# Optimization experiments

Hardware: AMD Instinct MI355X
Metric: run time of the kernel (lower is better)

The kernel has to match this reference:

```python
import jax, jax.numpy as jnp
import numpy as np

# Qwen3 MoE sparse block reference.
# E experts, top-k routing with softmax probs, normalized top-k weights,
# gated-SiLU expert MLPs (gate/up H->I, down I->H), weighted scatter-combine.
E, K, H, I = 8, 2, 2048, 768
B, S = 2, 2048


def setup_inputs() -> dict:
    key = jax.random.key(0)
    k0, k1, k2, k3, k4 = jax.random.split(key, 5)
    hidden_states = jax.random.normal(k0, (B, S, H), jnp.float32)
    w_router = jax.random.normal(k1, (H, E), jnp.float32) * (1.0 / np.sqrt(H))
    wi0 = jax.random.normal(k2, (E, H, I), jnp.float32) * 0.02  # gate proj
    wi1 = jax.random.normal(k3, (E, H, I), jnp.float32) * 0.02  # up proj
    wo = jax.random.normal(k4, (E, I, H), jnp.float32) * 0.02   # down proj
    return {"hidden_states": hidden_states, "w_router": w_router,
            "wi0": wi0, "wi1": wi1, "wo": wo}


def _moe(hidden_states, w_router, wi0, wi1, wo):
    b, s, h = hidden_states.shape
    x = hidden_states.reshape(-1, h)                       # [T, H]
    router_logits = x @ w_router                           # [T, E]
    probs = jax.nn.softmax(router_logits.astype(jnp.float32), axis=-1)
    top_w, top_i = jax.lax.top_k(probs, K)                 # [T, K]
    # norm_topk_prob = True
    top_w = top_w / jnp.sum(top_w, axis=-1, keepdims=True)
    top_w = top_w.astype(x.dtype)
    # per-(expert, token) combine weight; zero for unrouted pairs -> same math
    # as the original gather/MLP/scatter-add over selected tokens.
    onehot = jax.nn.one_hot(top_i, E, dtype=x.dtype)       # [T, K, E]
    comb = jnp.einsum('tk,tke->et', top_w, onehot)         # [E, T]
    g = jax.nn.silu(jnp.einsum('th,ehi->eti', x, wi0))     # [E, T, I]
    u = jnp.einsum('th,ehi->eti', x, wi1)                  # [E, T, I]
    y = jnp.einsum('eti,eih->eth', g * u, wo)              # [E, T, H]
    out = jnp.einsum('et,eth->th', comb, y)                # [T, H]
    return out.reshape(b, s, h), router_logits


def reference(hidden_states, w_router, wi0, wi1, wo):
    return _moe(hidden_states, w_router, wi0, wi1, wo)
```

## Files before the change

### kernel.cpp

```cpp
#include <hip/hip_runtime.h>

#define T_TOK 4096
#define H_DIM 2048
#define I_DIM 768
#define E_NUM 8

typedef __attribute__((ext_vector_type(8))) short bf16x8;
typedef __attribute__((ext_vector_type(4))) float f32x4;

__device__ __forceinline__ unsigned short f2bf(float f) {
  union { float f; unsigned int u; } c; c.f = f;
  unsigned int r = c.u + 0x7fffu + ((c.u >> 16) & 1u);
  return (unsigned short)(r >> 16);
}

__device__ __forceinline__ void gl_lds16(const unsigned short* g, unsigned short* l) {
  __builtin_amdgcn_global_load_lds(
      (const __attribute__((address_space(1))) unsigned int*)g,
      (__attribute__((address_space(3))) unsigned int*)l, 16, 0, 0);
}

__global__ __launch_bounds__(256) void transpose_cast_kernel(
    const float* __restrict__ src, unsigned short* __restrict__ dst,
    int K, int N)
{
  const int e = blockIdx.z;
  const int kb = blockIdx.y * 64, nb = blockIdx.x * 64;
  src += (size_t)e * K * N + (size_t)kb * N + nb;
  dst += (size_t)e * N * K + (size_t)nb * K + kb;
  __shared__ float tile[64][65];
  const int tid = threadIdx.x;
  const int lr = tid >> 4, lc = (tid & 15) * 4;
#pragma unroll
  for (int it = 0; it < 4; ++it) {
    float4 v = *(const float4*)(src + (size_t)(lr + it * 16) * N + lc);
    tile[lr + it * 16][lc]     = v.x;
    tile[lr + it * 16][lc + 1] = v.y;
    tile[lr + it * 16][lc + 2] = v.z;
    tile[lr + it * 16][lc + 3] = v.w;
  }
  __syncthreads();
  const int wn = tid >> 2, wk = (tid & 3) * 16;
  union { uint4 u[2]; unsigned short h[16]; } o;
#pragma unroll
  for (int j = 0; j < 16; ++j) o.h[j] = f2bf(tile[wk + j][wn]);
  *(uint4*)(dst + (size_t)wn * K + wk)     = o.u[0];
  *(uint4*)(dst + (size_t)wn * K + wk + 8) = o.u[1];
}

#define RTOK 8
__global__ __launch_bounds__(256) void router_kernel(
    const float* __restrict__ x,
    const float* __restrict__ wr,
    unsigned short* __restrict__ xbf,
    float* __restrict__ logits_out,
    int* __restrict__ counts,
    int* __restrict__ entries,
    float* __restrict__ entry_w)
{
  const int tid = threadIdx.x;
  const int w = tid >> 6, lane = tid & 63;
  const int t0 = blockIdx.x * RTOK;
  const int hb = w * 512 + lane * 8;

  float wreg[8][8];
#pragma unroll
  for (int r = 0; r < 8; ++r) {
    *(float4*)&wreg[r][0] = *(const float4*)(wr + (size_t)(hb + r) * E_NUM);
    *(float4*)&wreg[r][4] = *(const float4*)(wr + (size_t)(hb + r) * E_NUM + 4);
  }

  __shared__ float red[RTOK][4][E_NUM];
  __shared__ float lg[RTOK][E_NUM];
  __shared__ int   ch_i[RTOK][2];
  __shared__ float ch_w[RTOK][2];

  for (int tt = 0; tt < RTOK; ++tt) {
    const int t = t0 + tt;
    float xv[8];
    *(float4*)&xv[0] = *(const float4*)(x + (size_t)t * H_DIM + hb);
    *(float4*)&xv[4] = *(const float4*)(x + (size_t)t * H_DIM + hb + 4);
    union { uint4 u; unsigned short h[8]; } o;
#pragma unroll
    for (int j = 0; j < 8; ++j) o.h[j] = f2bf(xv[j]);
    *(uint4*)(xbf + (size_t)t * H_DIM + hb) = o.u;

    float acc[E_NUM];
#pragma unroll
    for (int e = 0; e < E_NUM; ++e) acc[e] = 0.f;
#pragma unroll
    for (int r = 0; r < 8; ++r)
#pragma unroll
      for (int e = 0; e < E_NUM; ++e) acc[e] = fmaf(xv[r], wreg[r][e], acc[e]);
#pragma unroll
    for (int off = 32; off > 0; off >>= 1)
#pragma unroll
      for (int e = 0; e < E_NUM; ++e) acc[e] += __shfl_down(acc[e], off);
    if (lane == 0)
#pragma unroll
      for (int e = 0; e < E_NUM; ++e) red[tt][w][e] = acc[e];
  }
  __syncthreads();

  if (tid < RTOK * E_NUM) {
    const int tt = tid >> 3, e = tid & 7;
    float l = red[tt][0][e] + red[tt][1][e] + red[tt][2][e] + red[tt][3][e];
    lg[tt][e] = l;
    logits_out[(size_t)(t0 + tt) * E_NUM + e] = l;
  }
  __syncthreads();

  if (tid < RTOK) {
    const int tt = tid;
    float m1 = lg[tt][0]; int i1 = 0;
#pragma unroll
    for (int e = 1; e < E_NUM; ++e) if (lg[tt][e] > m1) { m1 = lg[tt][e]; i1 = e; }
    float m2 = -3.4e38f; int i2 = -1;
#pragma unroll
    for (int e = 0; e < E_NUM; ++e) if (e != i1 && lg[tt][e] > m2) { m2 = lg[tt][e]; i2 = e; }
    float w1 = 1.f / (1.f + __expf(m2 - m1));
    ch_i[tt][0] = i1; ch_i[tt][1] = i2;
    ch_w[tt][0] = w1; ch_w[tt][1] = 1.f - w1;
  }
  __syncthreads();

  if (tid < E_NUM) {
    const int e = tid;
    int cnt = 0;
#pragma unroll
    for (int tt = 0; tt < RTOK; ++tt) {
      if (ch_i[tt][0] == e) ++cnt;
      if (ch_i[tt][1] == e) ++cnt;
    }
    if (cnt > 0) {
      int base = atomicAdd(&counts[e], cnt);
      int pos = 0;
#pragma unroll
      for (int tt = 0; tt < RTOK; ++tt) {
#pragma unroll
        for (int k = 0; k < 2; ++k) {
          if (ch_i[tt][k] == e) {
            entries[e * T_TOK + base + pos] = (t0 + tt) * 2 + k;
            entry_w[e * T_TOK + base + pos] = ch_w[tt][k];
            ++pos;
          }
        }
      }
    }
  }
}

#define FRAG(arr, row, cb) \
  (*(const bf16x8*)(&(arr)[((row) << 6) + ((((cb)) ^ ((row) & 7)) << 3)]))

__global__ __launch_bounds__(256) void moe_up_kernel(
    const unsigned short* __restrict__ xbf,
    const unsigned short* __restrict__ wgt,
    const unsigned short* __restrict__ wut,
    const int* __restrict__ counts,
    const int* __restrict__ entries,
    unsigned short* __restrict__ act)
{
  const int e = blockIdx.z;
  const int cnt = counts[e];
  const int m0 = blockIdx.y * 128;
  if (m0 >= cnt) return;
  const int n0 = blockIdx.x * 64;
  const int tid = threadIdx.x;

  __shared__ __align__(16) unsigned short As[128 * 64];
  __shared__ __align__(16) unsigned short Bg[64 * 64];
  __shared__ __align__(16) unsigned short Bu[64 * 64];
  __shared__ int rowp[128];

  if (tid < 128) rowp[tid] = (m0 + tid < cnt) ? entries[e * T_TOK + m0 + tid] : -1;
  __syncthreads();

  const int w = tid >> 6, lane = tid & 63;
  const int lrow = lane >> 3, lchunk = lane & 7;
  const int jj = lchunk ^ lrow;

  const unsigned short* wg_e = wgt + (size_t)e * I_DIM * H_DIM + (size_t)n0 * H_DIM;
  const unsigned short* wu_e = wut + (size_t)e * I_DIM * H_DIM + (size_t)n0 * H_DIM;
  const unsigned short* gA[4];
  unsigned short* lA[4];
#pragma unroll
  for (int t4 = 0; t4 < 4; ++t4) {
    int r = (t4 * 4 + w) * 8 + lrow;
    int p = rowp[r];
    int tok = (p >= 0) ? (p >> 1) : 0;
    gA[t4] = xbf + (size_t)tok * H_DIM + jj * 8;
    lA[t4] = As + (t4 * 4 + w) * 512;
  }
  const unsigned short* gG[2]; const unsigned short* gU[2]; unsigned short* lG[2]; unsigned short* lU[2];
#pragma unroll
  for (int t2 = 0; t2 < 2; ++t2) {
    int r = (t2 * 4 + w) * 8 + lrow;
    gG[t2] = wg_e + (size_t)r * H_DIM + jj * 8;
    gU[t2] = wu_e + (size_t)r * H_DIM + jj * 8;
    lG[t2] = Bg + (t2 * 4 + w) * 512;
    lU[t2] = Bu + (t2 * 4 + w) * 512;
  }

  f32x4 accg[4][2], accu[4][2];
#pragma unroll
  for (int i = 0; i < 4; ++i)
#pragma unroll
    for (int j = 0; j < 2; ++j) {
      accg[i][j] = (f32x4){0.f, 0.f, 0.f, 0.f};
      accu[i][j] = (f32x4){0.f, 0.f, 0.f, 0.f};
    }

  const int msub = (w >> 1) * 64, nsub = (w & 1) * 32;
  const int fm = lane & 15, fq = lane >> 4;
  const int f7 = fm & 7;

  for (int kt = 0; kt < H_DIM; kt += 64) {
#pragma unroll
    for (int t4 = 0; t4 < 4; ++t4) gl_lds16(gA[t4] + kt, lA[t4]);
#pragma unroll
    for (int t2 = 0; t2 < 2; ++t2) {
      gl_lds16(gG[t2] + kt, lG[t2]);
      gl_lds16(gU[t2] + kt, lU[t2]);
    }
    __syncthreads();
#pragma unroll
    for (int ks = 0; ks < 64; ks += 32) {
      const int cb = (ks >> 3) + fq;
      bf16x8 a[4], bg[2], bu[2];
#pragma unroll
      for (int mi = 0; mi < 4; ++mi)
        a[mi] = FRAG(As, msub + mi * 16 + fm, cb);
#pragma unroll
      for (int ni = 0; ni < 2; ++ni) {
        bg[ni] = FRAG(Bg, nsub + ni * 16 + fm, cb);
        bu[ni] = FRAG(Bu, nsub + ni * 16 + fm, cb);
      }
#pragma unroll
      for (int mi = 0; mi < 4; ++mi)
#pragma unroll
        for (int ni = 0; ni < 2; ++ni) {
          accg[mi][ni] = __builtin_amdgcn_mfma_f32_16x16x32_bf16(a[mi], bg[ni], accg[mi][ni], 0, 0, 0);
          accu[mi][ni] = __builtin_amdgcn_mfma_f32_16x16x32_bf16(a[mi], bu[ni], accu[mi][ni], 0, 0, 0);
        }
    }
    __syncthreads();
  }
#pragma unroll
  for (int mi = 0; mi < 4; ++mi) {
#pragma unroll
    for (int r = 0; r < 4; ++r) {
      int ml = msub + mi * 16 + fq * 4 + r;
      int p = rowp[ml];
      if (p < 0) continue;
      size_t base = (size_t)p * I_DIM + n0 + nsub + fm;
#pragma unroll
      for (int ni = 0; ni < 2; ++ni) {
        float g = accg[mi][ni][r];
        float u = accu[mi][ni][r];
        float h = g / (1.f + __expf(-g)) * u;
        act[base + ni * 16] = f2bf(h);
      }
    }
  }
}

__global__ __launch_bounds__(256) void moe_down_kernel(
    const unsigned short* __restrict__ act,
    const unsigned short* __restrict__ wot,
    const int* __restrict__ counts,
    const int* __restrict__ entries,
    const float* __restrict__ entry_w,
    float* __restrict__ out)
{
  const int e = blockIdx.z;
  const int cnt = counts[e];
  const int m0 = blockIdx.y * 128;
  if (m0 >= cnt) return;
  const int n0 = blockIdx.x * 128;
  const int tid = threadIdx.x;

  __shared__ __align__(16) unsigned short As[128 * 64];
  __shared__ __align__(16) unsigned short Bt[128 * 64];
  __shared__ int rowp[128];
  __shared__ float roww[128];

  if (tid < 128) {
    int idx = m0 + tid;
    rowp[tid] = (idx < cnt) ? entries[e * T_TOK + idx] : -1;
    roww[tid] = (idx < cnt) ? entry_w[e * T_TOK + idx] : 0.f;
  }
  __syncthreads();

  const int w = tid >> 6, lane = tid & 63;
  const int lrow = lane >> 3, lchunk = lane & 7;
  const int jj = lchunk ^ lrow;

  const unsigned short* wo_e = wot + (size_t)e * H_DIM * I_DIM + (size_t)n0 * I_DIM;
  const unsigned short* gA[4]; unsigned short* lA[4];
  const unsigned short* gB[4]; unsigned short* lB[4];
#pragma unroll
  for (int t4 = 0; t4 < 4; ++t4) {
    int r = (t4 * 4 + w) * 8 + lrow;
    int p = rowp[r];
    int pr = (p >= 0) ? p : 0;
    gA[t4] = act + (size_t)pr * I_DIM + jj * 8;
    lA[t4] = As + (t4 * 4 + w) * 512;
    gB[t4] = wo_e + (size_t)r * I_DIM + jj * 8;
    lB[t4] = Bt + (t4 * 4 + w) * 512;
  }

  f32x4 acc[4][4];
#pragma unroll
  for (int i = 0; i < 4; ++i)
#pragma unroll
    for (int j = 0; j < 4; ++j) acc[i][j] = (f32x4){0.f, 0.f, 0.f, 0.f};

  const int msub = (w >> 1) * 64, nsub = (w & 1) * 64;
  const int fm = lane & 15, fq = lane >> 4;

  for (int kt = 0; kt < I_DIM; kt += 64) {
#pragma unroll
    for (int t4 = 0; t4 < 4; ++t4) {
      gl_lds16(gA[t4] + kt, lA[t4]);
      gl_lds16(gB[t4] + kt, lB[t4]);
    }
    __syncthreads();
#pragma unroll
    for (int ks = 0; ks < 64; ks += 32) {
      const int cb = (ks >> 3) + fq;
      bf16x8 a[4], b[4];
#pragma unroll
      for (int mi = 0; mi < 4; ++mi)
        a[mi] = FRAG(As, msub + mi * 16 + fm, cb);
#pragma unroll
      for (int ni = 0; ni < 4; ++ni)
        b[ni] = FRAG(Bt, nsub + ni * 16 + fm, cb);
#pragma unroll
      for (int mi = 0; mi < 4; ++mi)
#pragma unroll
        for (int ni = 0; ni < 4; ++ni)
          acc[mi][ni] = __builtin_amdgcn_mfma_f32_16x16x32_bf16(a[mi], b[ni], acc[mi][ni], 0, 0, 0);
    }
    __syncthreads();
  }
#pragma unroll
  for (int mi = 0; mi < 4; ++mi) {
#pragma unroll
    for (int r = 0; r < 4; ++r) {
      int ml = msub + mi * 16 + fq * 4 + r;
      int p = rowp[ml];
      if (p < 0) continue;
      float wt = roww[ml];
      float* dst = out + (size_t)(p >> 1) * H_DIM + n0 + nsub + fm;
#pragma unroll
      for (int ni = 0; ni < 4; ++ni)
        atomicAdd(dst + ni * 16, acc[mi][ni][r] * wt);
    }
  }
}

extern "C" void kernel_launch(void* const* d_in, const int* in_sizes, int n_in,
                              void* d_out, int out_size, void* d_ws, size_t ws_size,
                              hipStream_t stream) {
  const float* x   = (const float*)d_in[0];
  const float* wr  = (const float*)d_in[1];
  const float* wi0 = (const float*)d_in[2];
  const float* wi1 = (const float*)d_in[3];
  const float* wo  = (const float*)d_in[4];
  float* out = (float*)d_out;
  float* logits_out = out + (size_t)T_TOK * H_DIM;

  char* w = (char*)d_ws;
  int* counts    = (int*)w;
  int* entries   = (int*)(w + 64);
  float* entry_w = (float*)(w + 64 + (size_t)E_NUM * T_TOK * 4);
  size_t off = 64 + 2 * (size_t)E_NUM * T_TOK * 4;
  unsigned short* xbf = (unsigned short*)(w + off); off += (size_t)T_TOK * H_DIM * 2;
  unsigned short* wgt = (unsigned short*)(w + off); off += (size_t)E_NUM * H_DIM * I_DIM * 2;
  unsigned short* wut = (unsigned short*)(w + off); off += (size_t)E_NUM * H_DIM * I_DIM * 2;
  unsigned short* wot = (unsigned short*)(w + off); off += (size_t)E_NUM * H_DIM * I_DIM * 2;
  unsigned short* act = (unsigned short*)(w + off);

  hipMemsetAsync(d_out, 0, (size_t)T_TOK * H_DIM * sizeof(float), stream);
  hipMemsetAsync(counts, 0, 64, stream);
  transpose_cast_kernel<<<dim3(I_DIM / 64, H_DIM / 64, E_NUM), 256, 0, stream>>>(
      wi0, wgt, H_DIM, I_DIM);
  transpose_cast_kernel<<<dim3(I_DIM / 64, H_DIM / 64, E_NUM), 256, 0, stream>>>(
      wi1, wut, H_DIM, I_DIM);
  transpose_cast_kernel<<<dim3(H_DIM / 64, I_DIM / 64, E_NUM), 256, 0, stream>>>(
      wo, wot, I_DIM, H_DIM);
  router_kernel<<<T_TOK / RTOK, 256, 0, stream>>>(x, wr, xbf, logits_out, counts, entries, entry_w);
  moe_up_kernel<<<dim3(I_DIM / 64, T_TOK / 128, E_NUM), 256, 0, stream>>>(
      xbf, wgt, wut, counts, entries, act);
  moe_down_kernel<<<dim3(H_DIM / 128, T_TOK / 128, E_NUM), 256, 0, stream>>>(
      act, wot, counts, entries, entry_w, out);
}
```

Measured before the change: 413.9 us.

## Double-buffer LDS tiles in MoE up and down GEMM kernels

Both expert GEMM kernels now keep two LDS buffers for the A and B tiles. Each k-iteration issues the global-to-LDS loads for the next tile before running the MFMAs on the current one, with a prologue load before the loop. The aim is to hide global load latency behind matrix math instead of stalling at a barrier right after each load. In exchange LDS use per block roughly doubles to about 64KB, which may cut how many blocks fit on a CU.

Result: no change. 410.3 us (-0.9%).

```diff
diff --git a/kernel.cpp b/kernel.cpp
--- a/kernel.cpp
+++ b/kernel.cpp
@@ -168,9 +168,9 @@
   const int n0 = blockIdx.x * 64;
   const int tid = threadIdx.x;
 
-  __shared__ __align__(16) unsigned short As[128 * 64];
-  __shared__ __align__(16) unsigned short Bg[64 * 64];
-  __shared__ __align__(16) unsigned short Bu[64 * 64];
+  __shared__ __align__(16) unsigned short As[2][128 * 64];
+  __shared__ __align__(16) unsigned short Bg[2][64 * 64];
+  __shared__ __align__(16) unsigned short Bu[2][64 * 64];
   __shared__ int rowp[128];
 
   if (tid < 128) rowp[tid] = (m0 + tid < cnt) ? entries[e * T_TOK + m0 + tid] : -1;
@@ -183,23 +183,23 @@
   const unsigned short* wg_e = wgt + (size_t)e * I_DIM * H_DIM + (size_t)n0 * H_DIM;
   const unsigned short* wu_e = wut + (size_t)e * I_DIM * H_DIM + (size_t)n0 * H_DIM;
   const unsigned short* gA[4];
-  unsigned short* lA[4];
+  int aoff[4];
 #pragma unroll
   for (int t4 = 0; t4 < 4; ++t4) {
     int r = (t4 * 4 + w) * 8 + lrow;
     int p = rowp[r];
     int tok = (p >= 0) ? (p >> 1) : 0;
     gA[t4] = xbf + (size_t)tok * H_DIM + jj * 8;
-    lA[t4] = As + (t4 * 4 + w) * 512;
-  }
-  const unsigned short* gG[2]; const unsigned short* gU[2]; unsigned short* lG[2]; unsigned short* lU[2];
+    aoff[t4] = (t4 * 4 + w) * 512;
+  }
+  const unsigned short* gG[2]; const unsigned short* gU[2];
+  int boff[2];
 #pragma unroll
   for (int t2 = 0; t2 < 2; ++t2) {
     int r = (t2 * 4 + w) * 8 + lrow;
     gG[t2] = wg_e + (size_t)r * H_DIM + jj * 8;
     gU[t2] = wu_e + (size_t)r * H_DIM + jj * 8;
-    lG[t2] = Bg + (t2 * 4 + w) * 512;
-    lU[t2] = Bu + (t2 * 4 + w) * 512;
+    boff[t2] = (t2 * 4 + w) * 512;
   }
 
   f32x4 accg[4][2], accu[4][2];
@@ -213,28 +213,42 @@
 
   const int msub = (w >> 1) * 64, nsub = (w & 1) * 32;
   const int fm = lane & 15, fq = lane >> 4;
-  const int f7 = fm & 7;
-
+
+#pragma unroll
+  for (int t4 = 0; t4 < 4; ++t4) gl_lds16(gA[t4], &As[0][aoff[t4]]);
+#pragma unroll
+  for (int t2 = 0; t2 < 2; ++t2) {
+    gl_lds16(gG[t2], &Bg[0][boff[t2]]);
+    gl_lds16(gU[t2], &Bu[0][boff[t2]]);
+  }
+  __syncthreads();
+
+  int cur = 0;
   for (int kt = 0; kt < H_DIM; kt += 64) {
-#pragma unroll
-    for (int t4 = 0; t4 < 4; ++t4) gl_lds16(gA[t4] + kt, lA[t4]);
-#pragma unroll
-    for (int t2 = 0; t2 < 2; ++t2) {
-      gl_lds16(gG[t2] + kt, lG[t2]);
-      gl_lds16(gU[t2] + kt, lU[t2]);
-    }
-    __syncthreads();
+    const int nxt = cur ^ 1;
+    if (kt + 64 < H_DIM) {
+#pragma unroll
+      for (int t4 = 0; t4 < 4; ++t4) gl_lds16(gA[t4] + kt + 64, &As[nxt][aoff[t4]]);
+#pragma unroll
+      for (int t2 = 0; t2 < 2; ++t2) {
+        gl_lds16(gG[t2] + kt + 64, &Bg[nxt][boff[t2]]);
+        gl_lds16(gU[t2] + kt + 64, &Bu[nxt][boff[t2]]);
+      }
+    }
+    const unsigned short* Ac  = As[cur];
+    const unsigned short* Bgc = Bg[cur];
+    const unsigned short* Buc = Bu[cur];
 #pragma unroll
     for (int ks = 0; ks < 64; ks += 32) {
       const int cb = (ks >> 3) + fq;
       bf16x8 a[4], bg[2], bu[2];
 #pragma unroll
       for (int mi = 0; mi < 4; ++mi)
-        a[mi] = FRAG(As, msub + mi * 16 + fm, cb);
+        a[mi] = FRAG(Ac, msub + mi * 16 + fm, cb);
 #pragma unroll
       for (int ni = 0; ni < 2; ++ni) {
-        bg[ni] = FRAG(Bg, nsub + ni * 16 + fm, cb);
-        bu[ni] = FRAG(Bu, nsub + ni * 16 + fm, cb);
+        bg[ni] = FRAG(Bgc, nsub + ni * 16 + fm, cb);
+        bu[ni] = FRAG(Buc, nsub + ni * 16 + fm, cb);
       }
 #pragma unroll
       for (int mi = 0; mi < 4; ++mi)
@@ -245,6 +259,7 @@
         }
     }
     __syncthreads();
+    cur = nxt;
   }
 #pragma unroll
   for (int mi = 0; mi < 4; ++mi) {
@@ -280,8 +295,8 @@
   const int n0 = blockIdx.x * 128;
   const int tid = threadIdx.x;
 
-  __shared__ __align__(16) unsigned short As[128 * 64];
-  __shared__ __align__(16) unsigned short Bt[128 * 64];
+  __shared__ __align__(16) unsigned short As[2][128 * 64];
+  __shared__ __align__(16) unsigned short Bt[2][128 * 64];
   __shared__ int rowp[128];
   __shared__ float roww[128];
 
@@ -297,17 +312,16 @@
   const int jj = lchunk ^ lrow;
 
   const unsigned short* wo_e = wot + (size_t)e * H_DIM * I_DIM + (size_t)n0 * I_DIM;
-  const unsigned short* gA[4]; unsigned short* lA[4];
-  const unsigned short* gB[4]; unsigned short* lB[4];
+  const unsigned short* gA[4]; const unsigned short* gB[4];
+  int off4[4];
 #pragma unroll
   for (int t4 = 0; t4 < 4; ++t4) {
     int r = (t4 * 4 + w) * 8 + lrow;
     int p = rowp[r];
     int pr = (p >= 0) ? p : 0;
     gA[t4] = act + (size_t)pr * I_DIM + jj * 8;
-    lA[t4] = As + (t4 * 4 + w) * 512;
     gB[t4] = wo_e + (size_t)r * I_DIM + jj * 8;
-    lB[t4] = Bt + (t4 * 4 + w) * 512;
+    off4[t4] = (t4 * 4 + w) * 512;
   }
 
   f32x4 acc[4][4];
@@ -319,23 +333,35 @@
   const int msub = (w >> 1) * 64, nsub = (w & 1) * 64;
   const int fm = lane & 15, fq = lane >> 4;
 
+#pragma unroll
+  for (int t4 = 0; t4 < 4; ++t4) {
+    gl_lds16(gA[t4], &As[0][off4[t4]]);
+    gl_lds16(gB[t4], &Bt[0][off4[t4]]);
+  }
+  __syncthreads();
+
+  int cur = 0;
   for (int kt = 0; kt < I_DIM; kt += 64) {
-#pragma unroll
-    for (int t4 = 0; t4 < 4; ++t4) {
-      gl_lds16(gA[t4] + kt, lA[t4]);
-      gl_lds16(gB[t4] + kt, lB[t4]);
-    }
-    __syncthreads();
+    const int nxt = cur ^ 1;
+    if (kt + 64 < I_DIM) {
+#pragma unroll
+      for (int t4 = 0; t4 < 4; ++t4) {
+        gl_lds16(gA[t4] + kt + 64, &As[nxt][off4[t4]]);
+        gl_lds16(gB[t4] + kt + 64, &Bt[nxt][off4[t4]]);
+      }
+    }
+    const unsigned short* Ac = As[cur];
+    const unsigned short* Bc = Bt[cur];
 #pragma unroll
     for (int ks = 0; ks < 64; ks += 32) {
       const int cb = (ks >> 3) + fq;
       bf16x8 a[4], b[4];
 #pragma unroll
       for (int mi = 0; mi < 4; ++mi)
-        a[mi] = FRAG(As, msub + mi * 16 + fm, cb);
+        a[mi] = FRAG(Ac, msub + mi * 16 + fm, cb);
 #pragma unroll
       for (int ni = 0; ni < 4; ++ni)
-        b[ni] = FRAG(Bt, nsub + ni * 16 + fm, cb);
+        b[ni] = FRAG(Bc, nsub + ni * 16 + fm, cb);
 #pragma unroll
       for (int mi = 0; mi < 4; ++mi)
 #pragma unroll
@@ -343,6 +369,7 @@
           acc[mi][ni] = __builtin_amdgcn_mfma_f32_16x16x32_bf16(a[mi], b[ni], acc[mi][ni], 0, 0, 0);
     }
     __syncthreads();
+    cur = nxt;
   }
 #pragma unroll
   for (int mi = 0; mi < 4; ++mi) {
```

## Flatten MoE GEMM grids into a compacted list of active expert tiles

Applied to the files above, without the earlier changes.

Replaces the 3D (n, m, expert) grid, which launched a block for every possible 128-row tile of every expert and exited most of them early, with a 1D grid over at most 72 M-blocks. Each block finds its expert and row offset with a prefix sum over the per-expert counts. This removes thousands of empty blocks and their scheduling cost, and packs the real work contiguously. The risk is that the fixed MAX_MB cap (total tiles across experts is at most 64+8) must cover all routings, and every block now reads all eight counts.

New measurement: 417.3 us. No clear change (+0.8%).

```diff
diff --git a/kernel.cpp b/kernel.cpp
--- a/kernel.cpp
+++ b/kernel.cpp
@@ -153,6 +153,8 @@
 #define FRAG(arr, row, cb) \
   (*(const bf16x8*)(&(arr)[((row) << 6) + ((((cb)) ^ ((row) & 7)) << 3)]))
 
+#define MAX_MB 72
+
 __global__ __launch_bounds__(256) void moe_up_kernel(
     const unsigned short* __restrict__ xbf,
     const unsigned short* __restrict__ wgt,
@@ -161,11 +163,19 @@
     const int* __restrict__ entries,
     unsigned short* __restrict__ act)
 {
-  const int e = blockIdx.z;
-  const int cnt = counts[e];
-  const int m0 = blockIdx.y * 128;
-  if (m0 >= cnt) return;
-  const int n0 = blockIdx.x * 64;
+  const int bid = blockIdx.x;
+  const int nb = bid % (I_DIM / 64);
+  const int mbl = bid / (I_DIM / 64);
+  int e = -1, m0 = 0, cnt = 0, cum = 0;
+#pragma unroll
+  for (int ee = 0; ee < E_NUM; ++ee) {
+    int c = counts[ee];
+    int nmb = (c + 127) >> 7;
+    if (e < 0 && mbl < cum + nmb) { e = ee; m0 = (mbl - cum) << 7; cnt = c; }
+    cum += nmb;
+  }
+  if (e < 0) return;
+  const int n0 = nb * 64;
   const int tid = threadIdx.x;
 
   __shared__ __align__(16) unsigned short As[128 * 64];
@@ -213,7 +223,6 @@
 
   const int msub = (w >> 1) * 64, nsub = (w & 1) * 32;
   const int fm = lane & 15, fq = lane >> 4;
-  const int f7 = fm & 7;
 
   for (int kt = 0; kt < H_DIM; kt += 64) {
 #pragma unroll
@@ -273,11 +282,19 @@
     const float* __restrict__ entry_w,
     float* __restrict__ out)
 {
-  const int e = blockIdx.z;
-  const int cnt = counts[e];
-  const int m0 = blockIdx.y * 128;
-  if (m0 >= cnt) return;
-  const int n0 = blockIdx.x * 128;
+  const int bid = blockIdx.x;
+  const int nb = bid % (H_DIM / 128);
+  const int mbl = bid / (H_DIM / 128);
+  int e = -1, m0 = 0, cnt = 0, cum = 0;
+#pragma unroll
+  for (int ee = 0; ee < E_NUM; ++ee) {
+    int c = counts[ee];
+    int nmb = (c + 127) >> 7;
+    if (e < 0 && mbl < cum + nmb) { e = ee; m0 = (mbl - cum) << 7; cnt = c; }
+    cum += nmb;
+  }
+  if (e < 0) return;
+  const int n0 = nb * 128;
   const int tid = threadIdx.x;
 
   __shared__ __align__(16) unsigned short As[128 * 64];
@@ -391,8 +408,8 @@
   transpose_cast_kernel<<<dim3(H_DIM / 64, I_DIM / 64, E_NUM), 256, 0, stream>>>(
       wo, wot, I_DIM, H_DIM);
   router_kernel<<<T_TOK / RTOK, 256, 0, stream>>>(x, wr, xbf, logits_out, counts, entries, entry_w);
-  moe_up_kernel<<<dim3(I_DIM / 64, T_TOK / 128, E_NUM), 256, 0, stream>>>(
+  moe_up_kernel<<<dim3(MAX_MB * (I_DIM / 64)), 256, 0, stream>>>(
       xbf, wgt, wut, counts, entries, act);
-  moe_down_kernel<<<dim3(H_DIM / 128, T_TOK / 128, E_NUM), 256, 0, stream>>>(
+  moe_down_kernel<<<dim3(MAX_MB * (H_DIM / 128)), 256, 0, stream>>>(
       act, wot, counts, entries, entry_w, out);
 }
```
